# Optimization experiments

Hardware: AMD Instinct MI355X
Metric: run time of the kernel (lower is better)

Reference implementation:

```python
import jax, jax.numpy as jnp
import numpy as np

B, SQ, SKV, D, H = 4, 2048, 2048, 1024, 16
DH = D // H  # 64


def setup_inputs() -> dict:
    key = jax.random.key(0)
    ks = jax.random.split(key, 8)
    s = 0.02  # realistic init scale for weights
    return {
        "query": jax.random.normal(ks[0], (B, SQ, D), dtype=jnp.float32),
        "value": jax.random.normal(ks[1], (B, SKV, D), dtype=jnp.float32),
        "wq": jax.random.normal(ks[2], (H, D, DH), dtype=jnp.float32) * s,
        "bq": jnp.zeros((H, DH), dtype=jnp.float32),
        "wk": jax.random.normal(ks[3], (H, D, DH), dtype=jnp.float32) * s,
        "bk": jnp.zeros((H, DH), dtype=jnp.float32),
        "wv": jax.random.normal(ks[4], (H, D, DH), dtype=jnp.float32) * s,
        "bv": jnp.zeros((H, DH), dtype=jnp.float32),
        "wo": jax.random.normal(ks[5], (D, D), dtype=jnp.float32) * s,
        "bo": jnp.zeros((D,), dtype=jnp.float32),
    }


def reference(query, value, wq, bq, wk, bk, wv, bv, wo, bo):
    # Batched equivalent of the per-head Dense loop: [B,S,D] x [H,D,DH] -> [B,H,S,DH]
    q = jnp.einsum("bsd,hde->bhse", query, wq) + bq[None, :, None, :]
    k = jnp.einsum("bsd,hde->bhse", value, wk) + bk[None, :, None, :]
    v = jnp.einsum("bsd,hde->bhse", value, wv) + bv[None, :, None, :]
    scale = 1.0 / jnp.sqrt(jnp.asarray(DH, dtype=q.dtype))
    scores = jnp.einsum("bhqe,bhke->bhqk", q, k) * scale  # [B,H,SQ,SKV]
    align = jax.nn.softmax(scores, axis=-1)
    heads = jnp.einsum("bhqk,bhke->bhqe", align, v)  # [B,H,SQ,DH]
    # concat heads along feature dim (head order preserved)
    heads = jnp.transpose(heads, (0, 2, 1, 3)).reshape(B, SQ, D)
    return heads @ wo + bo
```

## Files before the change

### kernel.cpp

```cpp
#include <hip/hip_runtime.h>
#include <stdint.h>

#define DEVI __device__ __forceinline__

typedef __bf16  bf16x8 __attribute__((ext_vector_type(8)));
typedef float   f32x4  __attribute__((ext_vector_type(4)));
typedef float   f32x16 __attribute__((ext_vector_type(16)));
typedef uint32_t u32x4 __attribute__((ext_vector_type(4)));
typedef uint32_t u32x2v __attribute__((ext_vector_type(2)));
typedef uint16_t u16x8 __attribute__((ext_vector_type(8)));
typedef uint16_t u16x4 __attribute__((ext_vector_type(4)));

static constexpr int BB = 4, SQL = 2048, SKVL = 2048, DMODEL = 1024, NH = 16;
static constexpr int MROWS = BB * SQL;
static constexpr int KD = DMODEL;

DEVI uint16_t f2bf(float x) {
  uint32_t u = __builtin_bit_cast(uint32_t, x);
  u += 0x7FFFu + ((u >> 16) & 1u);
  return (uint16_t)(u >> 16);
}
DEVI uint32_t cvt2bf(float a, float b) {
  __bf16 x = (__bf16)a, y = (__bf16)b;
  return (uint32_t)__builtin_bit_cast(uint16_t, x) |
         ((uint32_t)__builtin_bit_cast(uint16_t, y) << 16);
}
DEVI f32x4 mfma16(bf16x8 a, bf16x8 b, f32x4 c) {
  return __builtin_amdgcn_mfma_f32_16x16x32_bf16(a, b, c, 0, 0, 0);
}
DEVI f32x16 mfma32(bf16x8 a, bf16x8 b, f32x16 c) {
  return __builtin_amdgcn_mfma_f32_32x32x16_bf16(a, b, c, 0, 0, 0);
}
DEVI void gload16(const void* g, void* l) {
  __builtin_amdgcn_global_load_lds((__attribute__((address_space(1))) const void*)g,
                                   (__attribute__((address_space(3))) void*)l, 16, 0, 0);
}
DEVI bf16x8 ldread(const void* p) { return __builtin_bit_cast(bf16x8, *(const u32x4*)p); }
DEVI u32x2v plswap(uint32_t a, uint32_t b) {
  return __builtin_amdgcn_permlane32_swap(a, b, false, false);
}

__global__ __launch_bounds__(256) void k_cvt(const float* __restrict__ q, const float* __restrict__ v,
                                             const float* __restrict__ wq, const float* __restrict__ wk,
                                             const float* __restrict__ wv, const float* __restrict__ wo,
                                             uint16_t* __restrict__ aq, uint16_t* __restrict__ av,
                                             uint16_t* __restrict__ wt) {
  const int bx = blockIdx.x;
  const int tid = threadIdx.x;
  if (bx < 1024) {
    __shared__ float lds[64 * 65];
    const float* src; int rstride; size_t obase; int d0;
    if (bx < 768) {
      const int zz = bx >> 8, rem = bx & 255, h = rem >> 4, dt = rem & 15;
      d0 = dt * 64;
      src = ((zz == 0) ? wq : (zz == 1) ? wk : wv) + (size_t)h * 65536;
      rstride = 64;
      obase = (size_t)zz * 1048576 + (size_t)h * 64 * 1024;
    } else {
      const int idx = bx - 768, dt = idx >> 4, nt = idx & 15;
      d0 = dt * 64;
      src = wo + nt * 64;
      rstride = 1024;
      obase = (size_t)3 * 1048576 + (size_t)(nt * 64) * 1024;
    }
    const int e4 = (tid & 15) * 4, dl0 = tid >> 4;
    #pragma unroll
    for (int p = 0; p < 4; ++p) {
      const int dl = dl0 + p * 16;
      const float4 x = *(const float4*)(src + (size_t)(d0 + dl) * rstride + e4);
      float* row = &lds[dl * 65 + e4];
      row[0] = x.x; row[1] = x.y; row[2] = x.z; row[3] = x.w;
    }
    __syncthreads();
    const int er = tid >> 2, dp = tid & 3;
    uint16_t tmp[16];
    #pragma unroll
    for (int i = 0; i < 16; ++i) tmp[i] = f2bf(lds[(dp * 16 + i) * 65 + er]);
    uint16_t* orow = wt + obase + (size_t)er * 1024 + d0 + dp * 16;
    u16x8 o0, o1;
    #pragma unroll
    for (int j = 0; j < 8; ++j) { o0[j] = tmp[j]; o1[j] = tmp[8 + j]; }
    *(u16x8*)orow = o0;
    *(u16x8*)(orow + 8) = o1;
  } else {
    const int64_t n4 = (int64_t)MROWS * DMODEL / 4;
    for (int64_t i = (int64_t)(bx - 1024) * 256 + tid; i < 2 * n4; i += (int64_t)2048 * 256) {
      const bool second = (i >= n4);
      const int64_t j = second ? i - n4 : i;
      const float4 x = (second ? (const float4*)v : (const float4*)q)[j];
      u16x4 o = { f2bf(x.x), f2bf(x.y), f2bf(x.z), f2bf(x.w) };
      *(u16x4*)((second ? av : aq) + j * 4) = o;
    }
  }
}

__global__ __launch_bounds__(256) void k_gemm3(const uint16_t* __restrict__ Aq, const uint16_t* __restrict__ Av,
                                               const uint16_t* __restrict__ Wt,
                                               const float* __restrict__ bq, const float* __restrict__ bk,
                                               const float* __restrict__ bv,
                                               uint16_t* __restrict__ Qb, uint16_t* __restrict__ Kb,
                                               uint16_t* __restrict__ Vb, float qscale) {
  __shared__ __align__(16) uint16_t SM[4][128 * 64];
  const int tid = threadIdx.x;
  const int w = tid >> 6, ln = tid & 63;
  const int g = ln >> 4, lc = ln & 15;
  const int seg = blockIdx.y >> 3;
  const int m0 = blockIdx.x * 128, n0 = (blockIdx.y & 7) * 128;
  const uint16_t* A = (seg == 0) ? Aq : Av;
  const uint16_t* Bt = Wt + (size_t)seg * 1048576;
  const float* bias = (seg == 0) ? bq : (seg == 1) ? bk : bv;
  uint16_t* outp = (seg == 0) ? Qb : (seg == 1) ? Kb : Vb;
  const float oscale = (seg == 0) ? qscale : 1.0f;
  const int wm = (w >> 1) * 64, wn = (w & 1) * 64;
  const int srow = w * 32 + (ln >> 3);
  const int colp = (ln & 7) * 16;

  f32x4 acc[4][4] = {};

  auto stage = [&](int kt, int bs) {
    #pragma unroll
    for (int i = 0; i < 4; ++i) {
      const int row = srow + i * 8;
      const int colb = colp ^ ((row & 7) << 4);
      gload16((const char*)(A + (size_t)(m0 + row) * KD + kt * 64) + colb,
              (char*)&SM[bs][0] + w * 4096 + i * 1024);
      gload16((const char*)(Bt + (size_t)(n0 + row) * KD + kt * 64) + colb,
              (char*)&SM[2 + bs][0] + w * 4096 + i * 1024);
    }
  };

  stage(0, 0);
  asm volatile("s_waitcnt vmcnt(0)" ::: "memory");
  __builtin_amdgcn_s_barrier();
  __builtin_amdgcn_sched_barrier(0);

  int cur = 0;
  #pragma unroll 2
  for (int kt = 0; kt < KD / 64; ++kt) {
    if (kt + 1 < KD / 64) stage(kt + 1, cur ^ 1);
    const char* Ac = (const char*)&SM[cur][0];
    const char* Bc = (const char*)&SM[2 + cur][0];
    #pragma unroll
    for (int kk = 0; kk < 2; ++kk) {
      bf16x8 af[4], bfr[4];
      #pragma unroll
      for (int mt = 0; mt < 4; ++mt) {
        const int row = wm + mt * 16 + lc;
        af[mt] = ldread(Ac + row * 128 + ((kk * 64 + g * 16) ^ ((row & 7) << 4)));
      }
      #pragma unroll
      for (int nt = 0; nt < 4; ++nt) {
        const int row = wn + nt * 16 + lc;
        bfr[nt] = ldread(Bc + row * 128 + ((kk * 64 + g * 16) ^ ((row & 7) << 4)));
      }
      #pragma unroll
      for (int mt = 0; mt < 4; ++mt)
        #pragma unroll
        for (int nt = 0; nt < 4; ++nt)
          acc[mt][nt] = mfma16(af[mt], bfr[nt], acc[mt][nt]);
    }
    asm volatile("s_waitcnt vmcnt(0)" ::: "memory");
    __builtin_amdgcn_s_barrier();
    __builtin_amdgcn_sched_barrier(0);
    cur ^= 1;
  }

  uint16_t* ldc = &SM[0][0];
  #pragma unroll
  for (int nt = 0; nt < 4; ++nt) {
    const int n = n0 + wn + nt * 16 + lc;
    const float bv_ = bias[n];
    #pragma unroll
    for (int mt = 0; mt < 4; ++mt) {
      #pragma unroll
      for (int r = 0; r < 4; ++r) {
        const int row = wm + mt * 16 + g * 4 + r;
        ldc[row * 136 + wn + nt * 16 + lc] = f2bf((acc[mt][nt][r] + bv_) * oscale);
      }
    }
  }
  __syncthreads();
  const int bb = m0 >> 11;
  const int s_base = m0 & 2047;
  const int h0 = n0 >> 6;
  #pragma unroll
  for (int j = 0; j < 8; ++j) {
    const int idx = j * 256 + tid;
    const int row = idx >> 4, slot = idx & 15;
    const int h = h0 + (slot >> 3);
    const int e = (slot & 7) * 8;
    const u16x8 val = *(const u16x8*)(ldc + row * 136 + slot * 8);
    *(u16x8*)(outp + (((size_t)(bb * NH + h) * SQL) + s_base + row) * 64 + e) = val;
  }
}

__global__ __launch_bounds__(256) void k_gemmO(const uint16_t* __restrict__ A, const uint16_t* __restrict__ Bt,
                                               const float* __restrict__ bias, float* __restrict__ outp) {
  __shared__ __align__(16) uint16_t Al[2][128 * 64];
  __shared__ __align__(16) uint16_t Bl[2][128 * 64];
  const int tid = threadIdx.x;
  const int w = tid >> 6, ln = tid & 63;
  const int g = ln >> 4, lc = ln & 15;
  const int m0 = blockIdx.x * 128, n0 = blockIdx.y * 128;
  const int wm = (w >> 1) * 64, wn = (w & 1) * 64;
  const int srow = w * 32 + (ln >> 3);
  const int colp = (ln & 7) * 16;

  f32x4 acc[4][4] = {};

  auto stage = [&](int kt, int bs) {
    #pragma unroll
    for (int i = 0; i < 4; ++i) {
      const int row = srow + i * 8;
      const int colb = colp ^ ((row & 7) << 4);
      gload16((const char*)(A + (size_t)(m0 + row) * KD + kt * 64) + colb,
              (char*)&Al[bs][0] + w * 4096 + i * 1024);
      gload16((const char*)(Bt + (size_t)(n0 + row) * KD + kt * 64) + colb,
              (char*)&Bl[bs][0] + w * 4096 + i * 1024);
    }
  };

  stage(0, 0);
  asm volatile("s_waitcnt vmcnt(0)" ::: "memory");
  __builtin_amdgcn_s_barrier();
  __builtin_amdgcn_sched_barrier(0);

  int cur = 0;
  #pragma unroll 2
  for (int kt = 0; kt < KD / 64; ++kt) {
    if (kt + 1 < KD / 64) stage(kt + 1, cur ^ 1);
    const char* Ac = (const char*)&Al[cur][0];
    const char* Bc = (const char*)&Bl[cur][0];
    #pragma unroll
    for (int kk = 0; kk < 2; ++kk) {
      bf16x8 af[4], bfr[4];
      #pragma unroll
      for (int mt = 0; mt < 4; ++mt) {
        const int row = wm + mt * 16 + lc;
        af[mt] = ldread(Ac + row * 128 + ((kk * 64 + g * 16) ^ ((row & 7) << 4)));
      }
      #pragma unroll
      for (int nt = 0; nt < 4; ++nt) {
        const int row = wn + nt * 16 + lc;
        bfr[nt] = ldread(Bc + row * 128 + ((kk * 64 + g * 16) ^ ((row & 7) << 4)));
      }
      #pragma unroll
      for (int mt = 0; mt < 4; ++mt)
        #pragma unroll
        for (int nt = 0; nt < 4; ++nt)
          acc[mt][nt] = mfma16(af[mt], bfr[nt], acc[mt][nt]);
    }
    asm volatile("s_waitcnt vmcnt(0)" ::: "memory");
    __builtin_amdgcn_s_barrier();
    __builtin_amdgcn_sched_barrier(0);
    cur ^= 1;
  }

  #pragma unroll
  for (int nt = 0; nt < 4; ++nt) {
    const int n = n0 + wn + nt * 16 + lc;
    const float bv_ = bias[n];
    #pragma unroll
    for (int mt = 0; mt < 4; ++mt) {
      #pragma unroll
      for (int r = 0; r < 4; ++r) {
        const int m = m0 + wm + mt * 16 + g * 4 + r;
        outp[(size_t)m * DMODEL + n] = acc[mt][nt][r] + bv_;
      }
    }
  }
}

__global__ __launch_bounds__(256, 3) void k_attn(const uint16_t* __restrict__ Qb,
                                                 const uint16_t* __restrict__ Kb,
                                                 const uint16_t* __restrict__ Vb,
                                                 uint16_t* __restrict__ Hd) {
  __shared__ __align__(16) uint16_t Kl[2][64 * 64];
  __shared__ __align__(16) uint16_t Vl[2][64 * 64];
  const int tid = threadIdx.x;
  const int w = tid >> 6, ln = tid & 63;
  const int ql = ln & 31, hi = ln >> 5;
  const int bsw = blockIdx.x;
  const int l = (bsw & 7) * 128 + (bsw >> 3);
  const int qx = l & 15, bh = l >> 4;
  const int q0 = qx * 128 + w * 32;

  const uint16_t* Qp = Qb + ((size_t)bh * SQL + q0 + ql) * 64;
  bf16x8 qf[4];
  #pragma unroll
  for (int s = 0; s < 4; ++s)
    qf[s] = __builtin_bit_cast(bf16x8, *(const u16x8*)(Qp + s * 16 + hi * 8));

  const uint16_t* Kbase = Kb + (size_t)bh * SKVL * 64;
  const uint16_t* Vbase = Vb + (size_t)bh * SKVL * 64;

  const int swl = (ln & 7) << 4;
  const int e0off = (hi << 4) ^ swl;
  const int rb = ql * 128;

  const int krow0 = w * 16 + (ln >> 3);
  const int kcolb = (((ln & 7) ^ (ln >> 3)) << 4);
  const int vkv = (tid & 31) * 2, ve0 = (tid >> 5) * 8;

  f32x16 acc0 = {}, acc1 = {};
  float lsum = 0.f;

  {
    #pragma unroll
    for (int i = 0; i < 2; ++i) {
      const int row = krow0 + i * 8;
      gload16((const char*)(Kbase + (size_t)row * 64) + kcolb,
              (char*)&Kl[0][0] + w * 2048 + i * 1024);
    }
    const u16x8 a = *(const u16x8*)(Vbase + (size_t)vkv * 64 + ve0);
    const u16x8 b = *(const u16x8*)(Vbase + (size_t)(vkv + 1) * 64 + ve0);
    #pragma unroll
    for (int i = 0; i < 8; ++i) {
      const int e = ve0 + i;
      *(uint32_t*)((char*)&Vl[0][0] + e * 128 + ((vkv * 2) ^ ((e & 7) << 4))) =
          (uint32_t)a[i] | ((uint32_t)b[i] << 16);
    }
  }
  __syncthreads();

  int cur = 0;
  for (int t = 0; t < SKVL / 64; ++t) {
    const bool pre = (t + 1 < SKVL / 64);
    u16x8 nv0, nv1;
    if (pre) {
      const uint16_t* Kc = Kbase + (size_t)(t + 1) * 4096;
      #pragma unroll
      for (int i = 0; i < 2; ++i) {
        const int row = krow0 + i * 8;
        gload16((const char*)(Kc + (size_t)row * 64) + kcolb,
                (char*)&Kl[cur ^ 1][0] + w * 2048 + i * 1024);
      }
      const uint16_t* Vc = Vbase + (size_t)(t + 1) * 4096;
      nv0 = *(const u16x8*)(Vc + (size_t)vkv * 64 + ve0);
      nv1 = *(const u16x8*)(Vc + (size_t)(vkv + 1) * 64 + ve0);
    }
    const char* Kc0 = (const char*)&Kl[cur][0];
    f32x16 s0 = {}, s1 = {};
    __builtin_amdgcn_s_setprio(1);
    #pragma unroll
    for (int s = 0; s < 4; ++s) {
      const int off = e0off ^ (s << 5);
      const bf16x8 k0 = ldread(Kc0 + rb + off);
      const bf16x8 k1 = ldread(Kc0 + 4096 + rb + off);
      s0 = mfma32(k0, qf[s], s0);
      s1 = mfma32(k1, qf[s], s1);
    }
    __builtin_amdgcn_s_setprio(0);
    float ps = 0.f;
    #pragma unroll
    for (int r = 0; r < 16; ++r) {
      s0[r] = __builtin_amdgcn_exp2f(s0[r]);
      s1[r] = __builtin_amdgcn_exp2f(s1[r]);
      ps += s0[r] + s1[r];
    }
    lsum += ps;
    uint32_t w32[2][4][2];
    #pragma unroll
    for (int c8 = 0; c8 < 4; ++c8) {
      #pragma unroll
      for (int p = 0; p < 2; ++p) {
        w32[0][c8][p] = cvt2bf(s0[4 * c8 + 2 * p], s0[4 * c8 + 2 * p + 1]);
        w32[1][c8][p] = cvt2bf(s1[4 * c8 + 2 * p], s1[4 * c8 + 2 * p + 1]);
      }
    }
    const char* Vc0 = (const char*)&Vl[cur][0];
    __builtin_amdgcn_s_setprio(1);
    #pragma unroll
    for (int u = 0; u < 4; ++u) {
      const int tt = u >> 1, ul = u & 1;
      const u32x2v e0 = plswap(w32[tt][2 * ul][0], w32[tt][2 * ul + 1][0]);
      const u32x2v e1 = plswap(w32[tt][2 * ul][1], w32[tt][2 * ul + 1][1]);
      u32x4 pj;
      pj[0] = e0[0]; pj[1] = e1[0]; pj[2] = e0[1]; pj[3] = e1[1];
      const bf16x8 pb = __builtin_bit_cast(bf16x8, pj);
      const int off = e0off ^ (u << 5);
      const bf16x8 v0 = ldread(Vc0 + rb + off);
      const bf16x8 v1 = ldread(Vc0 + 4096 + rb + off);
      acc0 = mfma32(v0, pb, acc0);
      acc1 = mfma32(v1, pb, acc1);
    }
    __builtin_amdgcn_s_setprio(0);
    if (pre) {
      #pragma unroll
      for (int i = 0; i < 8; ++i) {
        const int e = ve0 + i;
        *(uint32_t*)((char*)&Vl[cur ^ 1][0] + e * 128 + ((vkv * 2) ^ ((e & 7) << 4))) =
            (uint32_t)nv0[i] | ((uint32_t)nv1[i] << 16);
      }
    }
    __syncthreads();
    cur ^= 1;
  }
  {
    const float lt = lsum + __shfl_xor(lsum, 32);
    const float inv = __builtin_amdgcn_rcpf(lt);
    const int b = bh >> 4, h = bh & 15;
    uint16_t* op = Hd + ((size_t)(b * SQL + q0 + ql)) * DMODEL + h * 64;
    #pragma unroll
    for (int et = 0; et < 2; ++et) {
      #pragma unroll
      for (int r2 = 0; r2 < 8; ++r2) {
        const float v0 = (et ? acc1[2 * r2] : acc0[2 * r2]) * inv;
        const float v1 = (et ? acc1[2 * r2 + 1] : acc0[2 * r2 + 1]) * inv;
        const int e = et * 32 + 4 * hi + (r2 & 1) * 2 + (r2 >> 1) * 8;
        *(uint32_t*)(op + e) = cvt2bf(v0, v1);
      }
    }
  }
}

extern "C" void kernel_launch(void* const* d_in, const int* in_sizes, int n_in,
                              void* d_out, int out_size, void* d_ws, size_t ws_size,
                              hipStream_t stream) {
  const float* query = (const float*)d_in[0];
  const float* value = (const float*)d_in[1];
  const float* wq = (const float*)d_in[2];
  const float* bq = (const float*)d_in[3];
  const float* wk = (const float*)d_in[4];
  const float* bk = (const float*)d_in[5];
  const float* wv = (const float*)d_in[6];
  const float* bv = (const float*)d_in[7];
  const float* wo = (const float*)d_in[8];
  const float* bo = (const float*)d_in[9];

  const size_t SZ_ACT = (size_t)MROWS * DMODEL * 2;
  const size_t SZ_W   = (size_t)4 * DMODEL * DMODEL * 2;
  if (ws_size < 6 * SZ_ACT + SZ_W) return;

  char* ws = (char*)d_ws;
  uint16_t* Aq = (uint16_t*)ws;  ws += SZ_ACT;
  uint16_t* Av = (uint16_t*)ws;  ws += SZ_ACT;
  uint16_t* Wt = (uint16_t*)ws;  ws += SZ_W;
  uint16_t* Qb = (uint16_t*)ws;  ws += SZ_ACT;
  uint16_t* Kb = (uint16_t*)ws;  ws += SZ_ACT;
  uint16_t* Vb = (uint16_t*)ws;  ws += SZ_ACT;
  uint16_t* Hd = (uint16_t*)ws;  ws += SZ_ACT;

  const float QSCALE = 0.18033688011112042f;

  k_cvt<<<dim3(3072), dim3(256), 0, stream>>>(query, value, wq, wk, wv, wo, Aq, Av, Wt);
  k_gemm3<<<dim3(64, 24), dim3(256), 0, stream>>>(Aq, Av, Wt, bq, bk, bv, Qb, Kb, Vb, QSCALE);
  k_attn<<<dim3(1024), dim3(256), 0, stream>>>(Qb, Kb, Vb, Hd);
  k_gemmO<<<dim3(64, 8), dim3(256), 0, stream>>>(Hd, Wt + 3145728, bo, (float*)d_out);
}
```

Before: 204.1 us.

## Emit V transposed from projection GEMM and stage it with async loads

The QKV projection epilogue now writes V in a per-head transposed [e][kv] layout, going through an LDS transpose. The attention kernel can then stage V tiles with the same direct global-to-LDS async loads used for K. This replaces the per-iteration register loads, bf16 packing and scattered LDS writes it used to transpose V. The trade-off is strided 16-byte global writes in the GEMM epilogue and LDS bank conflicts from the transposed stores there.

```diff
diff --git a/kernel.cpp b/kernel.cpp
--- a/kernel.cpp
+++ b/kernel.cpp
@@ -99,7 +99,7 @@
                                                const float* __restrict__ bq, const float* __restrict__ bk,
                                                const float* __restrict__ bv,
                                                uint16_t* __restrict__ Qb, uint16_t* __restrict__ Kb,
-                                               uint16_t* __restrict__ Vb, float qscale) {
+                                               uint16_t* __restrict__ Vt, float qscale) {
   __shared__ __align__(16) uint16_t SM[4][128 * 64];
   const int tid = threadIdx.x;
   const int w = tid >> 6, ln = tid & 63;
@@ -109,7 +109,6 @@
   const uint16_t* A = (seg == 0) ? Aq : Av;
   const uint16_t* Bt = Wt + (size_t)seg * 1048576;
   const float* bias = (seg == 0) ? bq : (seg == 1) ? bk : bv;
-  uint16_t* outp = (seg == 0) ? Qb : (seg == 1) ? Kb : Vb;
   const float oscale = (seg == 0) ? qscale : 1.0f;
   const int wm = (w >> 1) * 64, wn = (w & 1) * 64;
   const int srow = w * 32 + (ln >> 3);
@@ -166,31 +165,58 @@
   }
 
   uint16_t* ldc = &SM[0][0];
-  #pragma unroll
-  for (int nt = 0; nt < 4; ++nt) {
-    const int n = n0 + wn + nt * 16 + lc;
-    const float bv_ = bias[n];
-    #pragma unroll
-    for (int mt = 0; mt < 4; ++mt) {
-      #pragma unroll
-      for (int r = 0; r < 4; ++r) {
-        const int row = wm + mt * 16 + g * 4 + r;
-        ldc[row * 136 + wn + nt * 16 + lc] = f2bf((acc[mt][nt][r] + bv_) * oscale);
-      }
-    }
-  }
-  __syncthreads();
   const int bb = m0 >> 11;
   const int s_base = m0 & 2047;
   const int h0 = n0 >> 6;
-  #pragma unroll
-  for (int j = 0; j < 8; ++j) {
-    const int idx = j * 256 + tid;
-    const int row = idx >> 4, slot = idx & 15;
-    const int h = h0 + (slot >> 3);
-    const int e = (slot & 7) * 8;
-    const u16x8 val = *(const u16x8*)(ldc + row * 136 + slot * 8);
-    *(u16x8*)(outp + (((size_t)(bb * NH + h) * SQL) + s_base + row) * 64 + e) = val;
+  if (seg != 2) {
+    #pragma unroll
+    for (int nt = 0; nt < 4; ++nt) {
+      const int n = n0 + wn + nt * 16 + lc;
+      const float bv_ = bias[n];
+      #pragma unroll
+      for (int mt = 0; mt < 4; ++mt) {
+        #pragma unroll
+        for (int r = 0; r < 4; ++r) {
+          const int row = wm + mt * 16 + g * 4 + r;
+          ldc[row * 136 + wn + nt * 16 + lc] = f2bf((acc[mt][nt][r] + bv_) * oscale);
+        }
+      }
+    }
+    __syncthreads();
+    uint16_t* outp = (seg == 0) ? Qb : Kb;
+    #pragma unroll
+    for (int j = 0; j < 8; ++j) {
+      const int idx = j * 256 + tid;
+      const int row = idx >> 4, slot = idx & 15;
+      const int h = h0 + (slot >> 3);
+      const int e = (slot & 7) * 8;
+      const u16x8 val = *(const u16x8*)(ldc + row * 136 + slot * 8);
+      *(u16x8*)(outp + (((size_t)(bb * NH + h) * SQL) + s_base + row) * 64 + e) = val;
+    }
+  } else {
+    #pragma unroll
+    for (int nt = 0; nt < 4; ++nt) {
+      const int n = n0 + wn + nt * 16 + lc;
+      const float bv_ = bias[n];
+      #pragma unroll
+      for (int mt = 0; mt < 4; ++mt) {
+        #pragma unroll
+        for (int r = 0; r < 4; ++r) {
+          const int row = wm + mt * 16 + g * 4 + r;
+          ldc[(wn + nt * 16 + lc) * 136 + row] = f2bf(acc[mt][nt][r] + bv_);
+        }
+      }
+    }
+    __syncthreads();
+    #pragma unroll
+    for (int j = 0; j < 8; ++j) {
+      const int idx = j * 256 + tid;
+      const int er = idx >> 4, slot = idx & 15;
+      const int h = h0 + (er >> 6);
+      const int e = er & 63;
+      const u16x8 val = *(const u16x8*)(ldc + er * 136 + slot * 8);
+      *(u16x8*)(Vt + ((size_t)(bb * NH + h) * 64 + e) * SKVL + s_base + slot * 8) = val;
+    }
   }
 }
 
@@ -273,7 +299,7 @@
 
 __global__ __launch_bounds__(256, 3) void k_attn(const uint16_t* __restrict__ Qb,
                                                  const uint16_t* __restrict__ Kb,
-                                                 const uint16_t* __restrict__ Vb,
+                                                 const uint16_t* __restrict__ Vt,
                                                  uint16_t* __restrict__ Hd) {
   __shared__ __align__(16) uint16_t Kl[2][64 * 64];
   __shared__ __align__(16) uint16_t Vl[2][64 * 64];
@@ -292,7 +318,7 @@
     qf[s] = __builtin_bit_cast(bf16x8, *(const u16x8*)(Qp + s * 16 + hi * 8));
 
   const uint16_t* Kbase = Kb + (size_t)bh * SKVL * 64;
-  const uint16_t* Vbase = Vb + (size_t)bh * SKVL * 64;
+  const uint16_t* Vtb = Vt + (size_t)bh * 64 * SKVL;
 
   const int swl = (ln & 7) << 4;
   const int e0off = (hi << 4) ^ swl;
@@ -300,44 +326,36 @@
 
   const int krow0 = w * 16 + (ln >> 3);
   const int kcolb = (((ln & 7) ^ (ln >> 3)) << 4);
-  const int vkv = (tid & 31) * 2, ve0 = (tid >> 5) * 8;
+  const int vslot = ((ln & 7) ^ (ln >> 3)) * 8;
 
   f32x16 acc0 = {}, acc1 = {};
   float lsum = 0.f;
 
-  {
-    #pragma unroll
-    for (int i = 0; i < 2; ++i) {
-      const int row = krow0 + i * 8;
-      gload16((const char*)(Kbase + (size_t)row * 64) + kcolb,
-              (char*)&Kl[0][0] + w * 2048 + i * 1024);
-    }
-    const u16x8 a = *(const u16x8*)(Vbase + (size_t)vkv * 64 + ve0);
-    const u16x8 b = *(const u16x8*)(Vbase + (size_t)(vkv + 1) * 64 + ve0);
-    #pragma unroll
-    for (int i = 0; i < 8; ++i) {
-      const int e = ve0 + i;
-      *(uint32_t*)((char*)&Vl[0][0] + e * 128 + ((vkv * 2) ^ ((e & 7) << 4))) =
-          (uint32_t)a[i] | ((uint32_t)b[i] << 16);
-    }
-  }
+  auto stageK = [&](int t, int buf) {
+    const uint16_t* Kc = Kbase + (size_t)t * 4096;
+    #pragma unroll
+    for (int i = 0; i < 2; ++i)
+      gload16((const char*)(Kc + (size_t)(krow0 + i * 8) * 64) + kcolb,
+              (char*)&Kl[buf][0] + w * 2048 + i * 1024);
+  };
+  auto stageV = [&](int t, int buf) {
+    const uint16_t* Vc = Vtb + (size_t)t * 64 + vslot;
+    #pragma unroll
+    for (int i = 0; i < 2; ++i)
+      gload16((const char*)(Vc + (size_t)(krow0 + i * 8) * SKVL),
+              (char*)&Vl[buf][0] + w * 2048 + i * 1024);
+  };
+
+  stageK(0, 0);
+  stageV(0, 0);
   __syncthreads();
 
   int cur = 0;
   for (int t = 0; t < SKVL / 64; ++t) {
     const bool pre = (t + 1 < SKVL / 64);
-    u16x8 nv0, nv1;
     if (pre) {
-      const uint16_t* Kc = Kbase + (size_t)(t + 1) * 4096;
-      #pragma unroll
-      for (int i = 0; i < 2; ++i) {
-        const int row = krow0 + i * 8;
-        gload16((const char*)(Kc + (size_t)row * 64) + kcolb,
-                (char*)&Kl[cur ^ 1][0] + w * 2048 + i * 1024);
-      }
-      const uint16_t* Vc = Vbase + (size_t)(t + 1) * 4096;
-      nv0 = *(const u16x8*)(Vc + (size_t)vkv * 64 + ve0);
-      nv1 = *(const u16x8*)(Vc + (size_t)(vkv + 1) * 64 + ve0);
+      stageK(t + 1, cur ^ 1);
+      stageV(t + 1, cur ^ 1);
     }
     const char* Kc0 = (const char*)&Kl[cur][0];
     f32x16 s0 = {}, s1 = {};
@@ -385,14 +403,6 @@
       acc1 = mfma32(v1, pb, acc1);
     }
     __builtin_amdgcn_s_setprio(0);
-    if (pre) {
-      #pragma unroll
-      for (int i = 0; i < 8; ++i) {
-        const int e = ve0 + i;
-        *(uint32_t*)((char*)&Vl[cur ^ 1][0] + e * 128 + ((vkv * 2) ^ ((e & 7) << 4))) =
-            (uint32_t)nv0[i] | ((uint32_t)nv1[i] << 16);
-      }
-    }
     __syncthreads();
     cur ^= 1;
   }
@@ -438,13 +448,13 @@
   uint16_t* Wt = (uint16_t*)ws;  ws += SZ_W;
   uint16_t* Qb = (uint16_t*)ws;  ws += SZ_ACT;
   uint16_t* Kb = (uint16_t*)ws;  ws += SZ_ACT;
-  uint16_t* Vb = (uint16_t*)ws;  ws += SZ_ACT;
+  uint16_t* Vtw = (uint16_t*)ws; ws += SZ_ACT;
   uint16_t* Hd = (uint16_t*)ws;  ws += SZ_ACT;
 
   const float QSCALE = 0.18033688011112042f;
 
   k_cvt<<<dim3(3072), dim3(256), 0, stream>>>(query, value, wq, wk, wv, wo, Aq, Av, Wt);
-  k_gemm3<<<dim3(64, 24), dim3(256), 0, stream>>>(Aq, Av, Wt, bq, bk, bv, Qb, Kb, Vb, QSCALE);
-  k_attn<<<dim3(1024), dim3(256), 0, stream>>>(Qb, Kb, Vb, Hd);
+  k_gemm3<<<dim3(64, 24), dim3(256), 0, stream>>>(Aq, Av, Wt, bq, bk, bv, Qb, Kb, Vtw, QSCALE);
+  k_attn<<<dim3(1024), dim3(256), 0, stream>>>(Qb, Kb, Vtw, Hd);
   k_gemmO<<<dim3(64, 8), dim3(256), 0, stream>>>(Hd, Wt + 3145728, bo, (float*)d_out);
 }
```

Result: faster. 198.3 us (-2.8%).
